# Kernel optimization log

Measured on AMD Instinct MI355X. Metric: run time of the kernel, lower is better.

Reference implementation:

```python
import jax, jax.numpy as jnp
import numpy as np

B, S, D, H, G = 64, 1024, 512, 1024, 4096  # G = 4*H


def setup_inputs() -> dict:
    key = jax.random.key(0)
    ks = jax.random.split(key, 9)
    s = lambda fan: 1.0 / np.sqrt(H)  # torch LSTMCell init scale
    return {
        "x": jax.random.normal(ks[0], (B, S, D), dtype=jnp.float32),
        "W_ih0": jax.random.uniform(ks[1], (G, D), jnp.float32, -s(D), s(D)),
        "W_hh0": jax.random.uniform(ks[2], (G, H), jnp.float32, -s(H), s(H)),
        "b_ih0": jax.random.uniform(ks[3], (G,), jnp.float32, -s(H), s(H)),
        "b_hh0": jax.random.uniform(ks[4], (G,), jnp.float32, -s(H), s(H)),
        "W_ih1": jax.random.uniform(ks[5], (G, H), jnp.float32, -s(H), s(H)),
        "W_hh1": jax.random.uniform(ks[6], (G, H), jnp.float32, -s(H), s(H)),
        "b_ih1": jax.random.uniform(ks[7], (G,), jnp.float32, -s(H), s(H)),
        "b_hh1": jax.random.uniform(ks[8], (G,), jnp.float32, -s(H), s(H)),
    }


def _lstm_cell(x, h, c, W_ih, W_hh, b_ih, b_hh):
    # gates ordered i, f, g, o as in torch.nn.LSTMCell
    gates = x @ W_ih.T + b_ih + h @ W_hh.T + b_hh  # [B, 4H]
    i, f, g, o = jnp.split(gates, 4, axis=-1)
    c_new = jax.nn.sigmoid(f) * c + jax.nn.sigmoid(i) * jnp.tanh(g)
    h_new = jax.nn.sigmoid(o) * jnp.tanh(c_new)
    return h_new, c_new


def reference(x, W_ih0, W_hh0, b_ih0, b_hh0, W_ih1, W_hh1, b_ih1, b_hh1):
    batch = x.shape[0]
    zeros = jnp.zeros((batch, H), dtype=x.dtype)

    def step(carry, x_t):
        h0, c0, h1, c1 = carry
        h0, c0 = _lstm_cell(x_t, h0, c0, W_ih0, W_hh0, b_ih0, b_hh0)
        h1, c1 = _lstm_cell(h0, h1, c1, W_ih1, W_hh1, b_ih1, b_hh1)
        return (h0, c0, h1, c1), (h1, c1)

    carry0 = (zeros, zeros, zeros, zeros)
    xs = jnp.swapaxes(x, 0, 1)  # [S, B, D]
    (h0, c0, h1, c1), (hs, cs) = jax.lax.scan(step, carry0, xs)
    out = jnp.swapaxes(hs, 0, 1)    # [B, S, H] top-layer h per step
    c_out = jnp.swapaxes(cs, 0, 1)  # [B, S, H] top-layer c per step
    return (out, c_out, h1, c1)
```

## Files before the change

### kernel.cpp

```cpp
#include <hip/hip_runtime.h>
#include <stdint.h>

#define B_   64
#define S_   1024
#define D_   512
#define H_   1024
#define G_   4096
#define NWG  256

using bf16x8 = __attribute__((ext_vector_type(8))) short;
using f32x16 = __attribute__((ext_vector_type(16))) float;

#define GRP_OFF   0
#define TOP_OFF   2048
#define GEN_OFF   2176
#define RING_OFF  4096
#define SLOT_BYTES 131072
#define BSUM_OFF  532480
#define BFRAG_OFF 1048576
#define B0_PER_WG 98304
#define B1_OFF    (BFRAG_OFF + 128*B0_PER_WG)
#define B1_PER_WG 131072

#define BLDS_BYTES 131072
#define SMEM_TOTAL 147968

#define COUT_OFF 67108864ll
#define HF_OFF   134217728ll
#define CF_OFF   134283264ll

__device__ __forceinline__ uint16_t f2bf(float f) {
  uint32_t u = __float_as_uint(f);
  u += 0x7FFFu + ((u >> 16) & 1u);
  return (uint16_t)(u >> 16);
}
__device__ __forceinline__ float sigf(float x)  { return 1.0f / (1.0f + __expf(-x)); }
__device__ __forceinline__ float tanhf_(float x){ return 2.0f / (1.0f + __expf(-2.0f * x)) - 1.0f; }

__global__ void prep_misc(const float* __restrict__ bih0, const float* __restrict__ bhh0,
                          const float* __restrict__ bih1, const float* __restrict__ bhh1,
                          char* __restrict__ ws) {
  int tid = blockIdx.x * 256 + threadIdx.x;
  if (tid < 132096) { ((uint32_t*)ws)[tid] = 0u; return; }
  int i = tid - 132096;
  if (i < 8192) {
    int L = i >> 12, g = i & 4095;
    float v = L ? (bih1[g] + bhh1[g]) : (bih0[g] + bhh0[g]);
    ((float*)(ws + BSUM_OFF))[L * 4096 + g] = v;
  }
}

__global__ void prep_w(const float* __restrict__ Wih0, const float* __restrict__ Whh0,
                       const float* __restrict__ Wih1, const float* __restrict__ Whh1,
                       char* __restrict__ ws) {
  int tid = blockIdx.x * 256 + threadIdx.x;
  if (tid >= 7340032) return;
  uint32_t* dst = (uint32_t*)(ws + BFRAG_OFF);
  int layer, wg, ks, lane, jp;
  if (tid < 3145728) { layer = 0; wg = tid / 24576; int rem = tid % 24576; ks = rem >> 8; int r2 = rem & 255; lane = r2 >> 2; jp = r2 & 3; }
  else { int t2 = tid - 3145728; layer = 1; wg = t2 / 32768; int rem = t2 % 32768; ks = rem >> 8; int r2 = rem & 255; lane = r2 >> 2; jp = r2 & 3; }
  int n = lane & 31;
  int row = (n >> 3) * 1024 + wg * 8 + (n & 7);
  int k = ks * 16 + ((lane >> 5) << 3) + jp * 2;
  float w0, w1;
  if (!layer) {
    if (k < 512) { w0 = Wih0[row * 512 + k];          w1 = Wih0[row * 512 + k + 1]; }
    else         { w0 = Whh0[row * 1024 + k - 512];   w1 = Whh0[row * 1024 + k - 511]; }
  } else {
    if (k < 1024){ w0 = Wih1[row * 1024 + k];         w1 = Wih1[row * 1024 + k + 1]; }
    else         { w0 = Whh1[row * 1024 + k - 1024];  w1 = Whh1[row * 1024 + k - 1023]; }
  }
  dst[tid] = (uint32_t)f2bf(w0) | ((uint32_t)f2bf(w1) << 16);
}

__global__ void prep_x(const float* __restrict__ x, float* __restrict__ out) {
  int tid = blockIdx.x * 256 + threadIdx.x;
  if (tid >= 16777216) return;
  int t = tid >> 14;
  int sidx = tid & 16383;
  int jp = sidx & 3;
  int lane = (sidx >> 2) & 63;
  int mtks = sidx >> 8;
  int mt = mtks & 1, ks = mtks >> 1;
  int b = mt * 32 + (lane & 31);
  int k = ks * 16 + ((lane >> 5) << 3) + jp * 2;
  const float* xp = x + ((long)b * S_ + t) * D_ + k;
  uint32_t v = (uint32_t)f2bf(xp[0]) | ((uint32_t)f2bf(xp[1]) << 16);
  ((uint32_t*)(out + COUT_OFF))[(long)(sidx >> 10) * 1048576 + ((long)t << 10) + (sidx & 1023)] = v;
}

__global__ void __launch_bounds__(256) lstm_main(float* __restrict__ out, char* __restrict__ ws) {
  extern __shared__ char smem[];
  float (*red)[64][33] = (float (*)[64][33])(smem + BLDS_BYTES);

  const int tid = threadIdx.x;
  const int lane = tid & 63;
  const int wave = tid >> 6;
  const int wg = blockIdx.x;
  const int layer = wg >> 7;
  const int cw = wg & 127;
  const int mt = wave >> 1;
  const int kh = wave & 1;

  uint32_t* grp_cnt = (uint32_t*)(ws + GRP_OFF + (size_t)(wg >> 5) * 256);
  uint32_t* top_cnt = (uint32_t*)(ws + TOP_OFF);
  uint32_t* bar_gen = (uint32_t*)(ws + GEN_OFF);
  const float* bsum = (const float*)(ws + BSUM_OFF) + layer * G_;
  const char* bwg = ws + (layer ? (B1_OFF + (size_t)cw * B1_PER_WG)
                                : (BFRAG_OFF + (size_t)cw * B0_PER_WG));
  float* coutF = out + COUT_OFF;

  const int ksteps = layer ? 128 : 96;
  const int ksph = ksteps >> 1;

  {
    const int nchunk = ksteps << 6;
    for (int i = tid; i < nchunk; i += 256)
      *(bf16x8*)(smem + (size_t)i * 16) = *(const bf16x8*)(bwg + (size_t)i * 16);
  }
  __syncthreads();

  float cst0 = 0.f, cst1 = 0.f;

  for (int t = 0; t <= S_; ++t) {
    if (t) {
      __syncthreads();
      if (tid == 0) {
        __threadfence();
        uint32_t prev = __hip_atomic_fetch_add(grp_cnt, 1u, __ATOMIC_RELAXED, __HIP_MEMORY_SCOPE_AGENT);
        if (prev == (uint32_t)(t * 32 - 1)) {
          uint32_t p2 = __hip_atomic_fetch_add(top_cnt, 1u, __ATOMIC_RELAXED, __HIP_MEMORY_SCOPE_AGENT);
          if (p2 == (uint32_t)(t * 8 - 1)) {
            __hip_atomic_store(bar_gen, (uint32_t)t, __ATOMIC_RELEASE, __HIP_MEMORY_SCOPE_AGENT);
          }
        }
        while (__hip_atomic_load(bar_gen, __ATOMIC_RELAXED, __HIP_MEMORY_SCOPE_AGENT) < (uint32_t)t)
          __builtin_amdgcn_s_sleep(1);
        __threadfence();
      }
      __syncthreads();
    }
    const bool active = layer ? (t >= 1) : (t < S_);
    if (active) {
      const char* slotH0 = ws + RING_OFF + (size_t)((t - 1) & 1) * SLOT_BYTES;
      const char* slotH1 = ws + RING_OFF + (size_t)(2 + (t & 1)) * SLOT_BYTES;

      f32x16 acc = {};
#pragma unroll 8
      for (int s = 0; s < ksph; ++s) {
        const int ks = kh * ksph + s;
        const char* ap;
        if (layer == 0) {
          if (ks < 32) {
            int si = ((ks * 2 + mt) * 64 + lane) * 4;
            ap = (const char*)(coutF + (((long)(si >> 10)) << 20) + ((long)t << 10) + (si & 1023));
          } else {
            int k2 = ks - 32;
            ap = slotH0 + ((k2 * 2 + mt) * 64 + lane) * 16;
          }
        } else {
          if (ks < 64) {
            ap = slotH0 + ((ks * 2 + mt) * 64 + lane) * 16;
          } else {
            int k2 = ks - 64;
            ap = slotH1 + ((k2 * 2 + mt) * 64 + lane) * 16;
          }
        }
        bf16x8 av = *(const bf16x8*)ap;
        bf16x8 bv = *(const bf16x8*)(smem + (size_t)ks * 1024 + (size_t)lane * 16);
        acc = __builtin_amdgcn_mfma_f32_32x32x16_bf16(av, bv, acc, 0, 0, 0);
      }
      const int col = lane & 31;
      const int rbase = 4 * (lane >> 5);
#pragma unroll
      for (int r = 0; r < 16; ++r) {
        int row = (r & 3) + 8 * (r >> 2) + rbase;
        red[kh][mt * 32 + row][col] = acc[r];
      }
      __syncthreads();

      const int b = lane;
      const int bmt = b >> 5;
      char* pub = ws + RING_OFF + (size_t)((layer << 1) + ((layer ? (t - 1) : t) & 1)) * SLOT_BYTES;
#pragma unroll
      for (int r = 0; r < 2; ++r) {
        int cc = wave + 4 * r;
        int hc = cw * 8 + cc;
        float g0 = red[0][b][cc]      + red[1][b][cc]      + bsum[hc];
        float g1 = red[0][b][8 + cc]  + red[1][b][8 + cc]  + bsum[1024 + hc];
        float g2 = red[0][b][16 + cc] + red[1][b][16 + cc] + bsum[2048 + hc];
        float g3 = red[0][b][24 + cc] + red[1][b][24 + cc] + bsum[3072 + hc];
        float cprev = r ? cst1 : cst0;
        float cn = sigf(g1) * cprev + sigf(g0) * tanhf_(g2);
        float hn = sigf(g3) * tanhf_(cn);
        if (r) cst1 = cn; else cst0 = cn;
        int ksh = hc >> 4, rem = hc & 15;
        int laned = (b & 31) + ((rem >> 3) << 5);
        ((uint16_t*)pub)[((ksh * 2 + bmt) * 64 + laned) * 8 + (rem & 7)] = f2bf(hn);
        if (layer) {
          long s_ = t - 1;
          long idx = ((long)b << 20) + (s_ << 10) + hc;
          out[idx] = hn;
          out[COUT_OFF + idx] = cn;
          if (s_ == S_ - 1) {
            out[HF_OFF + ((long)b << 10) + hc] = hn;
            out[CF_OFF + ((long)b << 10) + hc] = cn;
          }
        }
      }
    }
  }
}

extern "C" void kernel_launch(void* const* d_in, const int* in_sizes, int n_in,
                              void* d_out, int out_size, void* d_ws, size_t ws_size,
                              hipStream_t stream) {
  const float* x    = (const float*)d_in[0];
  const float* Wih0 = (const float*)d_in[1];
  const float* Whh0 = (const float*)d_in[2];
  const float* bih0 = (const float*)d_in[3];
  const float* bhh0 = (const float*)d_in[4];
  const float* Wih1 = (const float*)d_in[5];
  const float* Whh1 = (const float*)d_in[6];
  const float* bih1 = (const float*)d_in[7];
  const float* bhh1 = (const float*)d_in[8];
  float* out = (float*)d_out;
  char* ws = (char*)d_ws;

  static bool attr_set = false;
  if (!attr_set) {
    (void)hipFuncSetAttribute((const void*)lstm_main,
                              hipFuncAttributeMaxDynamicSharedMemorySize, SMEM_TOTAL);
    attr_set = true;
  }

  hipLaunchKernelGGL(prep_misc, dim3((140288 + 255) / 256), dim3(256), 0, stream, bih0, bhh0, bih1, bhh1, ws);
  hipLaunchKernelGGL(prep_w,    dim3(7340032 / 256),        dim3(256), 0, stream, Wih0, Whh0, Wih1, Whh1, ws);
  hipLaunchKernelGGL(prep_x,    dim3(16777216 / 256),       dim3(256), 0, stream, x, out);

  void* args[] = { (void*)&out, (void*)&ws };
  hipLaunchCooperativeKernel((void*)lstm_main, dim3(NWG), dim3(256), args, SMEM_TOTAL, stream);
}
```

Before: 34.39 ms.

## Replace grid-barrier fences with agent-scope atomics and split MFMA accumulator

Result: faster. 29.81 ms (-13.3%).

```diff
diff --git a/kernel.cpp b/kernel.cpp
--- a/kernel.cpp
+++ b/kernel.cpp
@@ -36,6 +36,16 @@
 }
 __device__ __forceinline__ float sigf(float x)  { return 1.0f / (1.0f + __expf(-x)); }
 __device__ __forceinline__ float tanhf_(float x){ return 2.0f / (1.0f + __expf(-2.0f * x)) - 1.0f; }
+
+__device__ __forceinline__ void pub2(uint16_t* p, uint16_t v) {
+  __hip_atomic_store(p, v, __ATOMIC_RELAXED, __HIP_MEMORY_SCOPE_AGENT);
+}
+__device__ __forceinline__ bf16x8 ring_ld(const char* p) {
+  union { unsigned long long q[2]; bf16x8 v; } u;
+  u.q[0] = __hip_atomic_load((const unsigned long long*)p,       __ATOMIC_RELAXED, __HIP_MEMORY_SCOPE_AGENT);
+  u.q[1] = __hip_atomic_load((const unsigned long long*)(p + 8), __ATOMIC_RELAXED, __HIP_MEMORY_SCOPE_AGENT);
+  return u.v;
+}
 
 __global__ void prep_misc(const float* __restrict__ bih0, const float* __restrict__ bhh0,
                           const float* __restrict__ bih1, const float* __restrict__ bhh1,
@@ -112,6 +122,7 @@
 
   const int ksteps = layer ? 128 : 96;
   const int ksph = ksteps >> 1;
+  const int khalf = ksph >> 1;
 
   {
     const int nchunk = ksteps << 6;
@@ -124,19 +135,19 @@
 
   for (int t = 0; t <= S_; ++t) {
     if (t) {
+      asm volatile("s_waitcnt vmcnt(0)" ::: "memory");
       __syncthreads();
       if (tid == 0) {
-        __threadfence();
         uint32_t prev = __hip_atomic_fetch_add(grp_cnt, 1u, __ATOMIC_RELAXED, __HIP_MEMORY_SCOPE_AGENT);
         if (prev == (uint32_t)(t * 32 - 1)) {
           uint32_t p2 = __hip_atomic_fetch_add(top_cnt, 1u, __ATOMIC_RELAXED, __HIP_MEMORY_SCOPE_AGENT);
           if (p2 == (uint32_t)(t * 8 - 1)) {
-            __hip_atomic_store(bar_gen, (uint32_t)t, __ATOMIC_RELEASE, __HIP_MEMORY_SCOPE_AGENT);
+            __hip_atomic_store(bar_gen, (uint32_t)t, __ATOMIC_RELAXED, __HIP_MEMORY_SCOPE_AGENT);
           }
         }
         while (__hip_atomic_load(bar_gen, __ATOMIC_RELAXED, __HIP_MEMORY_SCOPE_AGENT) < (uint32_t)t)
           __builtin_amdgcn_s_sleep(1);
-        __threadfence();
+        asm volatile("" ::: "memory");
       }
       __syncthreads();
     }
@@ -145,37 +156,37 @@
       const char* slotH0 = ws + RING_OFF + (size_t)((t - 1) & 1) * SLOT_BYTES;
       const char* slotH1 = ws + RING_OFF + (size_t)(2 + (t & 1)) * SLOT_BYTES;
 
-      f32x16 acc = {};
+      f32x16 accA = {}, accB = {};
 #pragma unroll 8
       for (int s = 0; s < ksph; ++s) {
         const int ks = kh * ksph + s;
-        const char* ap;
+        bf16x8 av;
         if (layer == 0) {
           if (ks < 32) {
             int si = ((ks * 2 + mt) * 64 + lane) * 4;
-            ap = (const char*)(coutF + (((long)(si >> 10)) << 20) + ((long)t << 10) + (si & 1023));
+            av = *(const bf16x8*)(coutF + (((long)(si >> 10)) << 20) + ((long)t << 10) + (si & 1023));
           } else {
             int k2 = ks - 32;
-            ap = slotH0 + ((k2 * 2 + mt) * 64 + lane) * 16;
+            av = ring_ld(slotH0 + ((k2 * 2 + mt) * 64 + lane) * 16);
           }
         } else {
           if (ks < 64) {
-            ap = slotH0 + ((ks * 2 + mt) * 64 + lane) * 16;
+            av = ring_ld(slotH0 + ((ks * 2 + mt) * 64 + lane) * 16);
           } else {
             int k2 = ks - 64;
-            ap = slotH1 + ((k2 * 2 + mt) * 64 + lane) * 16;
+            av = ring_ld(slotH1 + ((k2 * 2 + mt) * 64 + lane) * 16);
           }
         }
-        bf16x8 av = *(const bf16x8*)ap;
         bf16x8 bv = *(const bf16x8*)(smem + (size_t)ks * 1024 + (size_t)lane * 16);
-        acc = __builtin_amdgcn_mfma_f32_32x32x16_bf16(av, bv, acc, 0, 0, 0);
+        if (s < khalf) accA = __builtin_amdgcn_mfma_f32_32x32x16_bf16(av, bv, accA, 0, 0, 0);
+        else           accB = __builtin_amdgcn_mfma_f32_32x32x16_bf16(av, bv, accB, 0, 0, 0);
       }
       const int col = lane & 31;
       const int rbase = 4 * (lane >> 5);
 #pragma unroll
       for (int r = 0; r < 16; ++r) {
         int row = (r & 3) + 8 * (r >> 2) + rbase;
-        red[kh][mt * 32 + row][col] = acc[r];
+        red[kh][mt * 32 + row][col] = accA[r] + accB[r];
       }
       __syncthreads();
 
@@ -196,7 +207,7 @@
         if (r) cst1 = cn; else cst0 = cn;
         int ksh = hc >> 4, rem = hc & 15;
         int laned = (b & 31) + ((rem >> 3) << 5);
-        ((uint16_t*)pub)[((ksh * 2 + bmt) * 64 + laned) * 8 + (rem & 7)] = f2bf(hn);
+        pub2(&((uint16_t*)pub)[((ksh * 2 + bmt) * 64 + laned) * 8 + (rem & 7)], f2bf(hn));
         if (layer) {
           long s_ = t - 1;
           long idx = ((long)b << 20) + (s_ << 10) + hc;
```
